# Optimization experiments

Hardware: AMD Instinct MI355X
Metric: run time of the kernel (lower is better)

The kernel has to match this reference:

```python
import jax, jax.numpy as jnp
import numpy as np

N, E, G = 100000, 3200000, 128
F, H = 9, 64


def _lin(key, fan_in, fan_out):
    s = 1.0 / np.sqrt(fan_in)
    k1, k2 = jax.random.split(key)
    W = jax.random.uniform(k1, (fan_in, fan_out), minval=-s, maxval=s, dtype=jnp.float32)
    b = jax.random.uniform(k2, (fan_out,), minval=-s, maxval=s, dtype=jnp.float32)
    return W, b


def setup_inputs() -> dict:
    key = jax.random.key(0)
    ks = jax.random.split(key, 16)
    x = jax.random.normal(ks[0], (N, F), dtype=jnp.float32)
    edge_index = jax.random.randint(ks[1], (2, E), 0, N, dtype=jnp.int64)
    edge_attr = jax.random.normal(ks[2], (E, 1), dtype=jnp.float32)
    batch = jnp.sort(jax.random.randint(ks[3], (N,), 0, G, dtype=jnp.int64))
    B_total = jax.random.uniform(ks[4], (G,), dtype=jnp.float32)
    terminal_mask = jax.random.randint(ks[5], (N,), 0, 2, dtype=jnp.int32)
    c_cost = jax.random.uniform(ks[6], (N,), dtype=jnp.float32)
    We1, be1 = _lin(ks[7], 1, F)   # GINEConv edge projection edge_dim->in_channels
    W1a, b1a = _lin(ks[8], F, H)
    W1b, b1b = _lin(ks[9], H, H)
    We2, be2 = _lin(ks[10], 1, H)
    W2a, b2a = _lin(ks[11], H, H)
    W2b, b2b = _lin(ks[12], H, H)
    Wr1, br1 = _lin(ks[13], H, H // 2)
    Wr2, br2 = _lin(ks[14], H // 2, 1)
    return dict(x=x, edge_index=edge_index, edge_attr=edge_attr, batch=batch,
                B_total=B_total, terminal_mask=terminal_mask, c_cost=c_cost,
                We1=We1, be1=be1, W1a=W1a, b1a=b1a, W1b=W1b, b1b=b1b,
                We2=We2, be2=be2, W2a=W2a, b2a=b2a, W2b=W2b, b2b=b2b,
                Wr1=Wr1, br1=br1, Wr2=Wr2, br2=br2)


def _gine_conv(h, src, dst, edge_attr, We, be, Wa, ba, Wb, bb):
    # GINEConv (eps=0): nn((1+eps)*x_i + sum_j ReLU(x_j + Lin(edge_attr)))
    ea = edge_attr @ We + be                      # [E, dim]
    msg = jax.nn.relu(h[src] + ea)                # gather + edge fuse + relu
    agg = jax.ops.segment_sum(msg, dst, num_segments=N)  # scatter-add
    z = h + agg
    z = jax.nn.relu(z @ Wa + ba)
    return jax.nn.relu(z @ Wb + bb)


def reference(x, edge_index, edge_attr, batch, B_total, terminal_mask, c_cost,
              We1, be1, W1a, b1a, W1b, b1b, We2, be2, W2a, b2a, W2b, b2b,
              Wr1, br1, Wr2, br2):
    src, dst = edge_index[0], edge_index[1]
    h = _gine_conv(x, src, dst, edge_attr, We1, be1, W1a, b1a, W1b, b1b)
    h = _gine_conv(h, src, dst, edge_attr, We2, be2, W2a, b2a, W2b, b2b)
    pi_raw = jax.nn.sigmoid(jax.nn.relu(h @ Wr1 + br1) @ Wr2 + br2)[:, 0]  # [N]
    pi_raw = pi_raw * (1.0 - terminal_mask.astype(pi_raw.dtype))
    node_expenses = pi_raw * c_cost
    total_expenses = jax.ops.segment_sum(node_expenses, batch, num_segments=B_total.shape[0])
    ratio = jnp.minimum(B_total[batch] / (total_expenses[batch] + 1e-12), 1.0)
    return pi_raw * ratio
```

## Files before the change

kernel.cpp:

```cpp
#include <hip/hip_runtime.h>
#include <hip/hip_fp16.h>
#include <math.h>

#define TPB 256
#define P_BLOCKS 512
#define BSHIFT 8
#define BINS_MAX 512

struct alignas(8)  h2x2 { __half2 a, b; };
struct alignas(16) h2x4 { __half2 a, b, c, d; };

typedef _Float16 f16;
typedef __attribute__((ext_vector_type(8))) _Float16 f16x8;
typedef __attribute__((ext_vector_type(4))) float f32x4;

#define MFMA16(a, b, c) __builtin_amdgcn_mfma_f32_16x16x32_f16(a, b, c, 0, 0, 0)

__global__ void __launch_bounds__(256) k_bhist(const int* __restrict__ dst,
                                               int* __restrict__ counts, int E, int B) {
  __shared__ int h[BINS_MAX];
  int t = threadIdx.x, blk = blockIdx.x;
  for (int i = t; i < B; i += TPB) h[i] = 0;
  __syncthreads();
  int chunk = (E + P_BLOCKS - 1) / P_BLOCKS;
  int s = blk * chunk, e = min(E, s + chunk);
  for (int i = s + t; i < e; i += TPB)
    atomicAdd(&h[__builtin_nontemporal_load(&dst[i]) >> BSHIFT], 1);
  __syncthreads();
  for (int i = t; i < B; i += TPB) counts[i * P_BLOCKS + blk] = h[i];
}

__global__ void k_scan_block(const int* __restrict__ deg, int* __restrict__ offs,
                             int* __restrict__ bsums, int n) {
  __shared__ int lds[256];
  int t = threadIdx.x, b = blockIdx.x;
  int base = b * 1024 + t * 4;
  int v0 = (base + 0 < n) ? deg[base + 0] : 0;
  int v1 = (base + 1 < n) ? deg[base + 1] : 0;
  int v2 = (base + 2 < n) ? deg[base + 2] : 0;
  int v3 = (base + 3 < n) ? deg[base + 3] : 0;
  int s = v0 + v1 + v2 + v3;
  lds[t] = s;
  __syncthreads();
  int acc = s;
  for (int off = 1; off < 256; off <<= 1) {
    int x = (t >= off) ? lds[t - off] : 0;
    __syncthreads();
    acc += x;
    lds[t] = acc;
    __syncthreads();
  }
  int excl = acc - s;
  if (base + 0 < n) offs[base + 0] = excl;
  if (base + 1 < n) offs[base + 1] = excl + v0;
  if (base + 2 < n) offs[base + 2] = excl + v0 + v1;
  if (base + 3 < n) offs[base + 3] = excl + v0 + v1 + v2;
  if (t == 255) bsums[b] = acc;
}

__global__ void k_scan_mid(int* __restrict__ bsums, int nb) {
  __shared__ int lds[256];
  int t = threadIdx.x;
  int v = (t < nb) ? bsums[t] : 0;
  lds[t] = v;
  __syncthreads();
  int acc = v;
  for (int off = 1; off < 256; off <<= 1) {
    int x = (t >= off) ? lds[t - off] : 0;
    __syncthreads();
    acc += x;
    lds[t] = acc;
    __syncthreads();
  }
  if (t < nb) bsums[t] = acc - v;
}

__global__ void k_scan_add(int* __restrict__ offs, const int* __restrict__ bsums,
                           int n, int total) {
  int t = threadIdx.x, b = blockIdx.x;
  int add = bsums[b];
  int base = b * 1024 + t * 4;
#pragma unroll
  for (int j = 0; j < 4; ++j)
    if (base + j < n) offs[base + j] += add;
  if (b == 0 && t == 0) offs[n] = total;
}

__global__ void __launch_bounds__(256) k_bfill(const int* __restrict__ src,
                                               const int* __restrict__ dst,
                                               const float* __restrict__ attr,
                                               const int* __restrict__ offs,
                                               int2* __restrict__ ebuf, int E, int B) {
  __shared__ int cur[BINS_MAX];
  int t = threadIdx.x, blk = blockIdx.x;
  for (int i = t; i < B; i += TPB) cur[i] = offs[i * P_BLOCKS + blk];
  __syncthreads();
  int chunk = (E + P_BLOCKS - 1) / P_BLOCKS;
  int s = blk * chunk, e = min(E, s + chunk);
#pragma unroll 4
  for (int i = s + t; i < e; i += TPB) {
    int d = __builtin_nontemporal_load(&dst[i]);
    int sv = __builtin_nontemporal_load(&src[i]);
    float av = __builtin_nontemporal_load(&attr[i]);
    int bin = d >> BSHIFT;
    int pos = atomicAdd(&cur[bin], 1);
    ebuf[pos] = make_int2((sv << BSHIFT) | (d & ((1 << BSHIFT) - 1)), __float_as_int(av));
  }
}

__global__ void __launch_bounds__(256) k_bsort(const long long* __restrict__ ebuf,
                                               const int* __restrict__ offs,
                                               int2* __restrict__ csr,
                                               int* __restrict__ noffs,
                                               int N, int E) {
  __shared__ int hist[256];
  __shared__ int cursor[256];
  __shared__ int sc[256];
  int t = threadIdx.x, bkt = blockIdx.x;
  hist[t] = 0;
  __syncthreads();
  int s = offs[bkt * P_BLOCKS], e = offs[(bkt + 1) * P_BLOCKS];
#pragma unroll 4
  for (int i = s + t; i < e; i += TPB) {
    long long pv = __builtin_nontemporal_load(&ebuf[i]);
    int key = (int)(unsigned int)(pv & 0xffffffffLL);
    atomicAdd(&hist[key & 255], 1);
  }
  __syncthreads();
  int v = hist[t];
  int acc = v;
  sc[t] = v;
  __syncthreads();
  for (int off = 1; off < 256; off <<= 1) {
    int x = (t >= off) ? sc[t - off] : 0;
    __syncthreads();
    acc += x;
    sc[t] = acc;
    __syncthreads();
  }
  int base = s + acc - v;
  cursor[t] = base;
  int n = (bkt << BSHIFT) + t;
  if (n < N) noffs[n] = base;
  if (bkt == 0 && t == 0) noffs[N] = E;
  __syncthreads();
#pragma unroll 4
  for (int i = s + t; i < e; i += TPB) {
    long long pv = __builtin_nontemporal_load(&ebuf[i]);
    int key = (int)(unsigned int)(pv & 0xffffffffLL);
    int attr = (int)(unsigned int)(((unsigned long long)pv) >> 32);
    int pos = atomicAdd(&cursor[key & 255], 1);
    csr[pos] = make_int2(((unsigned int)key) >> BSHIFT, attr);
  }
}

__global__ void __launch_bounds__(256) k_agg1(
    const float* __restrict__ x, const int2* __restrict__ csr,
    const int* __restrict__ noffs, const float* __restrict__ We1,
    const float* __restrict__ be1, float* __restrict__ u1, int N) {
  int t = blockIdx.x * TPB + threadIdx.x;
  int node = t >> 4, f = t & 15;
  if (node >= N || f >= 9) return;
  int o0 = noffs[node], o1 = noffs[node + 1];
  float we = We1[f], be = be1[f];
  float acc = 0.f;
  int e = o0;
  for (; e + 3 < o1; e += 4) {
    int2 p0 = csr[e], p1 = csr[e + 1], p2 = csr[e + 2], p3 = csr[e + 3];
    float v0 = x[p0.x * 9 + f] + fmaf(__int_as_float(p0.y), we, be);
    float v1 = x[p1.x * 9 + f] + fmaf(__int_as_float(p1.y), we, be);
    float v2 = x[p2.x * 9 + f] + fmaf(__int_as_float(p2.y), we, be);
    float v3 = x[p3.x * 9 + f] + fmaf(__int_as_float(p3.y), we, be);
    acc += fmaxf(v0, 0.f) + fmaxf(v1, 0.f) + fmaxf(v2, 0.f) + fmaxf(v3, 0.f);
  }
  for (; e < o1; ++e) {
    int2 p = csr[e];
    acc += fmaxf(x[p.x * 9 + f] + fmaf(__int_as_float(p.y), we, be), 0.f);
  }
  u1[node * 9 + f] = x[node * 9 + f] + acc;
}

__global__ void __launch_bounds__(256) k_agg2(
    const __half* __restrict__ h1, const long long* __restrict__ csr,
    const int* __restrict__ noffs, const float* __restrict__ We2,
    const float* __restrict__ be2, float* __restrict__ u2, int N) {
  int gt = blockIdx.x * TPB + threadIdx.x;
  int node = gt >> 6;
  if (node >= N) return;
  int lane = gt & 63;
  int q = lane >> 3, c = lane & 7;
  float4 weA = *(const float4*)&We2[c * 8];
  float4 weB = *(const float4*)&We2[c * 8 + 4];
  float4 beA = *(const float4*)&be2[c * 8];
  float4 beB = *(const float4*)&be2[c * 8 + 4];
  int o0 = noffs[node], o1 = noffs[node + 1];
  float a0 = 0.f, a1 = 0.f, a2 = 0.f, a3 = 0.f, a4 = 0.f, a5 = 0.f, a6 = 0.f, a7 = 0.f;

#define AGG2_ACC(pv, v)                                                      \
  {                                                                          \
    float ea = __int_as_float((int)(unsigned int)(((unsigned long long)(pv)) >> 32)); \
    float2 f0 = __half22float2((v).a), f1 = __half22float2((v).b);           \
    float2 f2 = __half22float2((v).c), f3 = __half22float2((v).d);           \
    a0 += fmaxf(f0.x + fmaf(ea, weA.x, beA.x), 0.f);                         \
    a1 += fmaxf(f0.y + fmaf(ea, weA.y, beA.y), 0.f);                         \
    a2 += fmaxf(f1.x + fmaf(ea, weA.z, beA.z), 0.f);                         \
    a3 += fmaxf(f1.y + fmaf(ea, weA.w, beA.w), 0.f);                         \
    a4 += fmaxf(f2.x + fmaf(ea, weB.x, beB.x), 0.f);                         \
    a5 += fmaxf(f2.y + fmaf(ea, weB.y, beB.y), 0.f);                         \
    a6 += fmaxf(f3.x + fmaf(ea, weB.z, beB.z), 0.f);                         \
    a7 += fmaxf(f3.y + fmaf(ea, weB.w, beB.w), 0.f);                         \
  }

#define AGG2_ACCM(pv, v, m)                                                  \
  {                                                                          \
    float ea = __int_as_float((int)(unsigned int)(((unsigned long long)(pv)) >> 32)); \
    float2 f0 = __half22float2((v).a), f1 = __half22float2((v).b);           \
    float2 f2 = __half22float2((v).c), f3 = __half22float2((v).d);           \
    a0 += (m) ? fmaxf(f0.x + fmaf(ea, weA.x, beA.x), 0.f) : 0.f;             \
    a1 += (m) ? fmaxf(f0.y + fmaf(ea, weA.y, beA.y), 0.f) : 0.f;             \
    a2 += (m) ? fmaxf(f1.x + fmaf(ea, weA.z, beA.z), 0.f) : 0.f;             \
    a3 += (m) ? fmaxf(f1.y + fmaf(ea, weA.w, beA.w), 0.f) : 0.f;             \
    a4 += (m) ? fmaxf(f2.x + fmaf(ea, weB.x, beB.x), 0.f) : 0.f;             \
    a5 += (m) ? fmaxf(f2.y + fmaf(ea, weB.y, beB.y), 0.f) : 0.f;             \
    a6 += (m) ? fmaxf(f3.x + fmaf(ea, weB.z, beB.z), 0.f) : 0.f;             \
    a7 += (m) ? fmaxf(f3.y + fmaf(ea, weB.w, beB.w), 0.f) : 0.f;             \
  }

  int e = o0;
  for (; e + 32 <= o1; e += 32) {
    long long pv0 = __builtin_nontemporal_load(&csr[e + q]);
    long long pv1 = __builtin_nontemporal_load(&csr[e + 8 + q]);
    long long pv2 = __builtin_nontemporal_load(&csr[e + 16 + q]);
    long long pv3 = __builtin_nontemporal_load(&csr[e + 24 + q]);
    h2x4 v0 = *(const h2x4*)(h1 + (size_t)(int)(unsigned int)(pv0 & 0xffffffffLL) * 64 + c * 8);
    h2x4 v1 = *(const h2x4*)(h1 + (size_t)(int)(unsigned int)(pv1 & 0xffffffffLL) * 64 + c * 8);
    h2x4 v2 = *(const h2x4*)(h1 + (size_t)(int)(unsigned int)(pv2 & 0xffffffffLL) * 64 + c * 8);
    h2x4 v3 = *(const h2x4*)(h1 + (size_t)(int)(unsigned int)(pv3 & 0xffffffffLL) * 64 + c * 8);
    AGG2_ACC(pv0, v0); AGG2_ACC(pv1, v1); AGG2_ACC(pv2, v2); AGG2_ACC(pv3, v3);
  }
  if (e < o1) {
    int last = o1 - 1;
    int i0 = e + q;      bool m0 = i0 < o1; i0 = m0 ? i0 : last;
    int i1 = e + 8 + q;  bool m1 = i1 < o1; i1 = m1 ? i1 : last;
    int i2 = e + 16 + q; bool m2 = i2 < o1; i2 = m2 ? i2 : last;
    int i3 = e + 24 + q; bool m3 = i3 < o1; i3 = m3 ? i3 : last;
    long long pv0 = __builtin_nontemporal_load(&csr[i0]);
    long long pv1 = __builtin_nontemporal_load(&csr[i1]);
    long long pv2 = __builtin_nontemporal_load(&csr[i2]);
    long long pv3 = __builtin_nontemporal_load(&csr[i3]);
    h2x4 v0 = *(const h2x4*)(h1 + (size_t)(int)(unsigned int)(pv0 & 0xffffffffLL) * 64 + c * 8);
    h2x4 v1 = *(const h2x4*)(h1 + (size_t)(int)(unsigned int)(pv1 & 0xffffffffLL) * 64 + c * 8);
    h2x4 v2 = *(const h2x4*)(h1 + (size_t)(int)(unsigned int)(pv2 & 0xffffffffLL) * 64 + c * 8);
    h2x4 v3 = *(const h2x4*)(h1 + (size_t)(int)(unsigned int)(pv3 & 0xffffffffLL) * 64 + c * 8);
    AGG2_ACCM(pv0, v0, m0); AGG2_ACCM(pv1, v1, m1);
    AGG2_ACCM(pv2, v2, m2); AGG2_ACCM(pv3, v3, m3);
  }
#undef AGG2_ACC
#undef AGG2_ACCM

  a0 += __shfl_xor(a0, 8, 64); a0 += __shfl_xor(a0, 16, 64); a0 += __shfl_xor(a0, 32, 64);
  a1 += __shfl_xor(a1, 8, 64); a1 += __shfl_xor(a1, 16, 64); a1 += __shfl_xor(a1, 32, 64);
  a2 += __shfl_xor(a2, 8, 64); a2 += __shfl_xor(a2, 16, 64); a2 += __shfl_xor(a2, 32, 64);
  a3 += __shfl_xor(a3, 8, 64); a3 += __shfl_xor(a3, 16, 64); a3 += __shfl_xor(a3, 32, 64);
  a4 += __shfl_xor(a4, 8, 64); a4 += __shfl_xor(a4, 16, 64); a4 += __shfl_xor(a4, 32, 64);
  a5 += __shfl_xor(a5, 8, 64); a5 += __shfl_xor(a5, 16, 64); a5 += __shfl_xor(a5, 32, 64);
  a6 += __shfl_xor(a6, 8, 64); a6 += __shfl_xor(a6, 16, 64); a6 += __shfl_xor(a6, 32, 64);
  a7 += __shfl_xor(a7, 8, 64); a7 += __shfl_xor(a7, 16, 64); a7 += __shfl_xor(a7, 32, 64);

  if (q == 0) {
    h2x4 sf = *(const h2x4*)(h1 + (size_t)node * 64 + c * 8);
    float2 s0 = __half22float2(sf.a), s1 = __half22float2(sf.b);
    float2 s2 = __half22float2(sf.c), s3 = __half22float2(sf.d);
    float4 oA, oB;
    oA.x = s0.x + a0; oA.y = s0.y + a1; oA.z = s1.x + a2; oA.w = s1.y + a3;
    oB.x = s2.x + a4; oB.y = s2.y + a5; oB.z = s3.x + a6; oB.w = s3.y + a7;
    *(float4*)&u2[(size_t)node * 64 + c * 8] = oA;
    *(float4*)&u2[(size_t)node * 64 + c * 8 + 4] = oB;
  }
}

__global__ void __launch_bounds__(256) k_mlp9(
    const float* __restrict__ uin, const float* __restrict__ Wa,
    const float* __restrict__ ba, const float* __restrict__ Wb,
    const float* __restrict__ bb, __half* __restrict__ hout, int N) {
  constexpr int KIN = 9;
  __shared__ float ls_in[64 * KIN];
  __shared__ float ls_z[64 * 65];
  __shared__ float ls_w[64 * 64];
  __shared__ float ls_b[128];
  const int t = threadIdx.x;
  const int n0 = blockIdx.x * 64;

  for (int i = t; i < 64 * KIN; i += TPB) {
    int r = i / KIN, c = i % KIN;
    int g = n0 + r;
    ls_in[i] = (g < N) ? uin[g * KIN + c] : 0.f;
  }
  for (int i = t; i < KIN * 64; i += TPB) ls_w[i] = Wa[i];
  if (t < 64) { ls_b[t] = ba[t]; ls_b[64 + t] = bb[t]; }
  __syncthreads();

  const int of = (t & 15) * 4, nb = (t >> 4) * 4;
  float acc[4][4];
#pragma unroll
  for (int i = 0; i < 4; ++i)
#pragma unroll
    for (int j = 0; j < 4; ++j) acc[i][j] = 0.f;

  for (int k = 0; k < KIN; ++k) {
    float4 w = *(const float4*)&ls_w[k * 64 + of];
#pragma unroll
    for (int ni = 0; ni < 4; ++ni) {
      float uv = ls_in[(nb + ni) * KIN + k];
      acc[ni][0] += uv * w.x; acc[ni][1] += uv * w.y;
      acc[ni][2] += uv * w.z; acc[ni][3] += uv * w.w;
    }
  }
#pragma unroll
  for (int ni = 0; ni < 4; ++ni)
#pragma unroll
    for (int oi = 0; oi < 4; ++oi)
      ls_z[(nb + ni) * 65 + of + oi] = fmaxf(acc[ni][oi] + ls_b[of + oi], 0.f);
  __syncthreads();
  for (int i = t; i < 4096; i += TPB) ls_w[i] = Wb[i];
  __syncthreads();

#pragma unroll
  for (int i = 0; i < 4; ++i)
#pragma unroll
    for (int j = 0; j < 4; ++j) acc[i][j] = 0.f;
  for (int k = 0; k < 64; ++k) {
    float4 w = *(const float4*)&ls_w[k * 64 + of];
#pragma unroll
    for (int ni = 0; ni < 4; ++ni) {
      float zv = ls_z[(nb + ni) * 65 + k];
      acc[ni][0] += zv * w.x; acc[ni][1] += zv * w.y;
      acc[ni][2] += zv * w.z; acc[ni][3] += zv * w.w;
    }
  }
#pragma unroll
  for (int ni = 0; ni < 4; ++ni) {
    int n = n0 + nb + ni;
    if (n < N) {
      float ox = fmaxf(acc[ni][0] + ls_b[64 + of + 0], 0.f);
      float oy = fmaxf(acc[ni][1] + ls_b[64 + of + 1], 0.f);
      float oz = fmaxf(acc[ni][2] + ls_b[64 + of + 2], 0.f);
      float ow = fmaxf(acc[ni][3] + ls_b[64 + of + 3], 0.f);
      h2x2 hv;
      hv.a = __float22half2_rn(make_float2(ox, oy));
      hv.b = __float22half2_rn(make_float2(oz, ow));
      *(h2x2*)(hout + (size_t)n * 64 + of) = hv;
    }
  }
}

__device__ __forceinline__ void splitf8(const float* v, f16x8& h, f16x8& l) {
#pragma unroll
  for (int j = 0; j < 8; ++j) {
    float x = v[j];
    f16 hh = (f16)x;
    h[j] = hh;
    l[j] = (f16)(x - (float)hh);
  }
}

__device__ __forceinline__ void pack_w(const float* __restrict__ W, int Ntiles, int nslots,
                                       f16* hi, f16* lo, int t) {
  int lane = t & 63;
  int kg = lane >> 4, m = lane & 15;
  int Nout = Ntiles * 16;
  for (int s = t >> 6; s < nslots; s += 4) {
    int ks = s / Ntiles, nt = s - ks * Ntiles;
    int kbase = ks * 32 + kg * 8;
    int n = nt * 16 + m;
    float v[8];
#pragma unroll
    for (int j = 0; j < 8; ++j) v[j] = W[(kbase + j) * Nout + n];
    f16x8 h, l;
    splitf8(v, h, l);
    *(f16x8*)&hi[(s * 64 + lane) * 8] = h;
    *(f16x8*)&lo[(s * 64 + lane) * 8] = l;
  }
}

__global__ void __launch_bounds__(256) k_mlp_ro(
    const float* __restrict__ uin, const float* __restrict__ Wa,
    const float* __restrict__ ba, const float* __restrict__ Wb,
    const float* __restrict__ bb, const float* __restrict__ Wr1,
    const float* __restrict__ br1, const float* __restrict__ Wr2,
    const float* __restrict__ br2, const int* __restrict__ tmask,
    float* __restrict__ pi, int N) {
  __shared__ __align__(16) f16 wf1h[4096], wf1l[4096];
  __shared__ __align__(16) f16 wf2h[4096], wf2l[4096];
  __shared__ __align__(16) f16 wfrh[2048], wfrl[2048];
  __shared__ float ls_z[64 * 65];
  __shared__ float ls_ba[64], ls_bb[64], ls_br1[32], ls_w2[32];
  const int t = threadIdx.x;
  const int n0 = blockIdx.x * 64;

  pack_w(Wa, 4, 8, wf1h, wf1l, t);
  pack_w(Wb, 4, 8, wf2h, wf2l, t);
  pack_w(Wr1, 2, 4, wfrh, wfrl, t);
  if (t < 64) { ls_ba[t] = ba[t]; ls_bb[t] = bb[t]; }
  else if (t < 96) { ls_br1[t - 64] = br1[t - 64]; ls_w2[t - 64] = Wr2[t - 64]; }
  __syncthreads();

  const int w = t >> 6, lane = t & 63;
  const int m = lane & 15, kg = lane >> 4;

  int row = n0 + w * 16 + m;
  row = min(row, N - 1);
  const float* ar = uin + (size_t)row * 64 + kg * 8;
  float av0[8], av1[8];
  {
    f32x4 p0 = *(const f32x4*)ar;
    f32x4 p1 = *(const f32x4*)(ar + 4);
    f32x4 p2 = *(const f32x4*)(ar + 32);
    f32x4 p3 = *(const f32x4*)(ar + 36);
#pragma unroll
    for (int j = 0; j < 4; ++j) {
      av0[j] = p0[j]; av0[4 + j] = p1[j];
      av1[j] = p2[j]; av1[4 + j] = p3[j];
    }
  }
  f16x8 a0h, a0l, a1h, a1l;
  splitf8(av0, a0h, a0l);
  splitf8(av1, a1h, a1l);

  f32x4 acc[4];
#pragma unroll
  for (int nt = 0; nt < 4; ++nt) { f32x4 z4 = {0.f, 0.f, 0.f, 0.f}; acc[nt] = z4; }
#pragma unroll
  for (int nt = 0; nt < 4; ++nt) {
#pragma unroll
    for (int ks = 0; ks < 2; ++ks) {
      int s = ks * 4 + nt;
      f16x8 bh = *(const f16x8*)&wf1h[(s * 64 + lane) * 8];
      f16x8 bl = *(const f16x8*)&wf1l[(s * 64 + lane) * 8];
      f16x8 ah = ks ? a1h : a0h;
      f16x8 al = ks ? a1l : a0l;
      acc[nt] = MFMA16(ah, bh, acc[nt]);
      acc[nt] = MFMA16(al, bh, acc[nt]);
      acc[nt] = MFMA16(ah, bl, acc[nt]);
    }
  }
#pragma unroll
  for (int nt = 0; nt < 4; ++nt)
#pragma unroll
    for (int r = 0; r < 4; ++r)
      ls_z[(w * 16 + kg * 4 + r) * 65 + nt * 16 + m] = fmaxf(acc[nt][r] + ls_ba[nt * 16 + m], 0.f);
  __syncthreads();

  const float* zr = &ls_z[(size_t)(w * 16 + m) * 65 + kg * 8];
  {
    float zv0[8], zv1[8];
#pragma unroll
    for (int j = 0; j < 8; ++j) { zv0[j] = zr[j]; zv1[j] = zr[32 + j]; }
    splitf8(zv0, a0h, a0l);
    splitf8(zv1, a1h, a1l);
  }
#pragma unroll
  for (int nt = 0; nt < 4; ++nt) { f32x4 z4 = {0.f, 0.f, 0.f, 0.f}; acc[nt] = z4; }
#pragma unroll
  for (int nt = 0; nt < 4; ++nt) {
#pragma unroll
    for (int ks = 0; ks < 2; ++ks) {
      int s = ks * 4 + nt;
      f16x8 bh = *(const f16x8*)&wf2h[(s * 64 + lane) * 8];
      f16x8 bl = *(const f16x8*)&wf2l[(s * 64 + lane) * 8];
      f16x8 ah = ks ? a1h : a0h;
      f16x8 al = ks ? a1l : a0l;
      acc[nt] = MFMA16(ah, bh, acc[nt]);
      acc[nt] = MFMA16(al, bh, acc[nt]);
      acc[nt] = MFMA16(ah, bl, acc[nt]);
    }
  }
  __syncthreads();
#pragma unroll
  for (int nt = 0; nt < 4; ++nt)
#pragma unroll
    for (int r = 0; r < 4; ++r)
      ls_z[(w * 16 + kg * 4 + r) * 65 + nt * 16 + m] = fmaxf(acc[nt][r] + ls_bb[nt * 16 + m], 0.f);
  __syncthreads();

  {
    float zv0[8], zv1[8];
#pragma unroll
    for (int j = 0; j < 8; ++j) { zv0[j] = zr[j]; zv1[j] = zr[32 + j]; }
    splitf8(zv0, a0h, a0l);
    splitf8(zv1, a1h, a1l);
  }
  f32x4 accr[2];
#pragma unroll
  for (int nt = 0; nt < 2; ++nt) { f32x4 z4 = {0.f, 0.f, 0.f, 0.f}; accr[nt] = z4; }
#pragma unroll
  for (int nt = 0; nt < 2; ++nt) {
#pragma unroll
    for (int ks = 0; ks < 2; ++ks) {
      int s = ks * 2 + nt;
      f16x8 bh = *(const f16x8*)&wfrh[(s * 64 + lane) * 8];
      f16x8 bl = *(const f16x8*)&wfrl[(s * 64 + lane) * 8];
      f16x8 ah = ks ? a1h : a0h;
      f16x8 al = ks ? a1l : a0l;
      accr[nt] = MFMA16(ah, bh, accr[nt]);
      accr[nt] = MFMA16(al, bh, accr[nt]);
      accr[nt] = MFMA16(ah, bl, accr[nt]);
    }
  }
  float b2 = br2[0];
#pragma unroll
  for (int r = 0; r < 4; ++r) {
    float v0 = fmaxf(accr[0][r] + ls_br1[m], 0.f) * ls_w2[m];
    float v1 = fmaxf(accr[1][r] + ls_br1[16 + m], 0.f) * ls_w2[16 + m];
    float tr = v0 + v1;
    tr += __shfl_xor(tr, 1, 64);
    tr += __shfl_xor(tr, 2, 64);
    tr += __shfl_xor(tr, 4, 64);
    tr += __shfl_xor(tr, 8, 64);
    if (m == 0) {
      int node = n0 + w * 16 + kg * 4 + r;
      if (node < N) {
        float sg = 1.f / (1.f + expf(-(tr + b2)));
        pi[node] = sg * (1.f - (float)tmask[node]);
      }
    }
  }
}

__global__ void k_grpsum(const float* __restrict__ pi, const float* __restrict__ c_cost,
                         const int* __restrict__ batch, float* __restrict__ exp_tot, int N) {
  __shared__ float lsf[256];
  __shared__ int lsi[256];
  int t = threadIdx.x;
  int i = blockIdx.x * TPB + t;
  bool valid = i < N;
  int g = valid ? batch[i] : 0;
  float v = valid ? pi[i] * c_cost[i] : 0.f;
  lsi[t] = valid ? g : 0x7fffffff;
  __syncthreads();
  for (int s = 128; s > 0; s >>= 1) { if (t < s) lsi[t] = min(lsi[t], lsi[t + s]); __syncthreads(); }
  int gmin = lsi[0];
  __syncthreads();
  lsi[t] = valid ? g : -1;
  __syncthreads();
  for (int s = 128; s > 0; s >>= 1) { if (t < s) lsi[t] = max(lsi[t], lsi[t + s]); __syncthreads(); }
  int gmax = lsi[0];
  __syncthreads();
  for (int gg = gmin; gg <= gmax; ++gg) {
    lsf[t] = (valid && g == gg) ? v : 0.f;
    __syncthreads();
    for (int s = 128; s > 0; s >>= 1) { if (t < s) lsf[t] += lsf[t + s]; __syncthreads(); }
    if (t == 0) atomicAdd(&exp_tot[gg], lsf[0]);
    __syncthreads();
  }
}

__global__ void k_final(const float* __restrict__ pi, const int* __restrict__ batch,
                        const float* __restrict__ B_total, const float* __restrict__ exp_tot,
                        float* __restrict__ out, int N) {
  int i = blockIdx.x * TPB + threadIdx.x;
  if (i < N) {
    int g = batch[i];
    float ratio = fminf(B_total[g] / (exp_tot[g] + 1e-12f), 1.f);
    out[i] = pi[i] * ratio;
  }
}

extern "C" void kernel_launch(void* const* d_in, const int* in_sizes, int n_in,
                              void* d_out, int out_size, void* d_ws, size_t ws_size,
                              hipStream_t stream) {
  const float* x     = (const float*)d_in[0];
  const int*   ei    = (const int*)d_in[1];
  const float* eattr = (const float*)d_in[2];
  const int*   batch = (const int*)d_in[3];
  const float* Btot  = (const float*)d_in[4];
  const int*   tmask = (const int*)d_in[5];
  const float* ccost = (const float*)d_in[6];
  const float* We1 = (const float*)d_in[7],  *be1 = (const float*)d_in[8];
  const float* W1a = (const float*)d_in[9],  *b1a = (const float*)d_in[10];
  const float* W1b = (const float*)d_in[11], *b1b = (const float*)d_in[12];
  const float* We2 = (const float*)d_in[13], *be2 = (const float*)d_in[14];
  const float* W2a = (const float*)d_in[15], *b2a = (const float*)d_in[16];
  const float* W2b = (const float*)d_in[17], *b2b = (const float*)d_in[18];
  const float* Wr1 = (const float*)d_in[19], *br1 = (const float*)d_in[20];
  const float* Wr2 = (const float*)d_in[21], *br2 = (const float*)d_in[22];
  float* out = (float*)d_out;

  const int N = in_sizes[0] / 9;
  const int E = in_sizes[2];
  const int G = in_sizes[4];
  const int* src = ei;
  const int* dst = ei + E;
  const int B = (N + (1 << BSHIFT) - 1) >> BSHIFT;
  const int nscan = B * P_BLOCKS;

  size_t cur = 0;
  auto alloc = [&](size_t elems) { size_t r = cur; cur += elems; cur = (cur + 63) & ~(size_t)63; return r; };
  char* wsb = (char*)d_ws;
  size_t o_exp    = alloc(G);
  size_t o_counts = alloc(nscan);
  size_t o_offs   = alloc(nscan + 1);
  size_t o_bsums  = alloc(256);
  size_t o_noffs  = alloc(N + 1);
  size_t o_csr    = alloc(2 * (size_t)E);
  size_t e_or_h   = (2 * (size_t)E > (size_t)N * 32) ? 2 * (size_t)E : (size_t)N * 32;
  size_t o_ebuf   = alloc(e_or_h);
  size_t o_u1     = alloc((size_t)N * 9);
  size_t o_u2     = alloc((size_t)N * 64);
  size_t o_pi     = alloc(N);
  (void)ws_size;

  float* exp_t  = (float*)wsb + o_exp;
  int*   counts = (int*)wsb + o_counts;
  int*   offs   = (int*)wsb + o_offs;
  int*   bsums  = (int*)wsb + o_bsums;
  int*   noffs  = (int*)wsb + o_noffs;
  int2*  csr    = (int2*)((int*)wsb + o_csr);
  int2*  ebuf   = (int2*)((int*)wsb + o_ebuf);
  __half* h1h   = (__half*)((int*)wsb + o_ebuf);
  float* u1     = (float*)wsb + o_u1;
  float* u2     = (float*)wsb + o_u2;
  float* pi     = (float*)wsb + o_pi;

  (void)hipMemsetAsync(exp_t, 0, (size_t)G * 4, stream);

  const int nb = (nscan + 1023) / 1024;

  k_bhist<<<P_BLOCKS, TPB, 0, stream>>>(dst, counts, E, B);
  k_scan_block<<<nb, TPB, 0, stream>>>(counts, offs, bsums, nscan);
  k_scan_mid<<<1, 256, 0, stream>>>(bsums, nb);
  k_scan_add<<<nb, TPB, 0, stream>>>(offs, bsums, nscan, E);
  k_bfill<<<P_BLOCKS, TPB, 0, stream>>>(src, dst, eattr, offs, ebuf, E, B);
  k_bsort<<<B, TPB, 0, stream>>>((const long long*)ebuf, offs, csr, noffs, N, E);

  k_agg1<<<((size_t)N * 16 + TPB - 1) / TPB, TPB, 0, stream>>>(x, csr, noffs, We1, be1, u1, N);
  k_mlp9<<<(N + 63) / 64, TPB, 0, stream>>>(u1, W1a, b1a, W1b, b1b, h1h, N);

  k_agg2<<<((size_t)N * 64 + TPB - 1) / TPB, TPB, 0, stream>>>(h1h, (const long long*)csr, noffs, We2, be2, u2, N);
  k_mlp_ro<<<(N + 63) / 64, TPB, 0, stream>>>(u2, W2a, b2a, W2b, b2b, Wr1, br1, Wr2, br2, tmask, pi, N);

  k_grpsum<<<(N + TPB - 1) / TPB, TPB, 0, stream>>>(pi, ccost, batch, exp_t, N);
  k_final<<<(N + TPB - 1) / TPB, TPB, 0, stream>>>(pi, batch, Btot, exp_t, out, N);
}
```

Baseline: 425.8 us.

## Port layer-1 MLP to split-fp16 MFMA and pack aggregation math into float2

The first-layer node MLP (9->64->64) is rewritten from a scalar LDS-tiled FP32 GEMM to MFMA 16x16x32 f16 instructions, splitting inputs and weights into hi/lo halves to keep near-fp32 accuracy. Separately, the layer-2 edge aggregation switches to two-wide float vectors so the compiler can emit packed FP32 fma/max/add. The MFMA path cuts scalar FMA work but adds split overhead and per-element half stores, and packed math depends on compiler codegen.

After: 419.2 us. Within noise of the previous version (-1.5%).

```diff
diff --git a/kernel.cpp b/kernel.cpp
--- a/kernel.cpp
+++ b/kernel.cpp
@@ -13,6 +13,7 @@
 typedef _Float16 f16;
 typedef __attribute__((ext_vector_type(8))) _Float16 f16x8;
 typedef __attribute__((ext_vector_type(4))) float f32x4;
+typedef __attribute__((ext_vector_type(2))) float f32x2;
 
 #define MFMA16(a, b, c) __builtin_amdgcn_mfma_f32_16x16x32_f16(a, b, c, 0, 0, 0)
 
@@ -189,41 +190,42 @@
   if (node >= N) return;
   int lane = gt & 63;
   int q = lane >> 3, c = lane & 7;
-  float4 weA = *(const float4*)&We2[c * 8];
-  float4 weB = *(const float4*)&We2[c * 8 + 4];
-  float4 beA = *(const float4*)&be2[c * 8];
-  float4 beB = *(const float4*)&be2[c * 8 + 4];
+  f32x2 weP[4], beP[4];
+#pragma unroll
+  for (int p = 0; p < 4; ++p) {
+    weP[p] = *(const f32x2*)&We2[c * 8 + p * 2];
+    beP[p] = *(const f32x2*)&be2[c * 8 + p * 2];
+  }
   int o0 = noffs[node], o1 = noffs[node + 1];
-  float a0 = 0.f, a1 = 0.f, a2 = 0.f, a3 = 0.f, a4 = 0.f, a5 = 0.f, a6 = 0.f, a7 = 0.f;
+  f32x2 A0 = {0.f, 0.f}, A1 = {0.f, 0.f}, A2 = {0.f, 0.f}, A3 = {0.f, 0.f};
+  const f32x2 z2 = {0.f, 0.f};
 
 #define AGG2_ACC(pv, v)                                                      \
   {                                                                          \
-    float ea = __int_as_float((int)(unsigned int)(((unsigned long long)(pv)) >> 32)); \
-    float2 f0 = __half22float2((v).a), f1 = __half22float2((v).b);           \
-    float2 f2 = __half22float2((v).c), f3 = __half22float2((v).d);           \
-    a0 += fmaxf(f0.x + fmaf(ea, weA.x, beA.x), 0.f);                         \
-    a1 += fmaxf(f0.y + fmaf(ea, weA.y, beA.y), 0.f);                         \
-    a2 += fmaxf(f1.x + fmaf(ea, weA.z, beA.z), 0.f);                         \
-    a3 += fmaxf(f1.y + fmaf(ea, weA.w, beA.w), 0.f);                         \
-    a4 += fmaxf(f2.x + fmaf(ea, weB.x, beB.x), 0.f);                         \
-    a5 += fmaxf(f2.y + fmaf(ea, weB.y, beB.y), 0.f);                         \
-    a6 += fmaxf(f3.x + fmaf(ea, weB.z, beB.z), 0.f);                         \
-    a7 += fmaxf(f3.y + fmaf(ea, weB.w, beB.w), 0.f);                         \
-  }
-
-#define AGG2_ACCM(pv, v, m)                                                  \
+    float eaf = __int_as_float((int)(unsigned int)(((unsigned long long)(pv)) >> 32)); \
+    f32x2 ea2 = {eaf, eaf};                                                  \
+    float2 q0 = __half22float2((v).a), q1 = __half22float2((v).b);           \
+    float2 q2 = __half22float2((v).c), q3 = __half22float2((v).d);           \
+    f32x2 g0 = {q0.x, q0.y}, g1 = {q1.x, q1.y};                              \
+    f32x2 g2 = {q2.x, q2.y}, g3 = {q3.x, q3.y};                              \
+    A0 += __builtin_elementwise_max(g0 + __builtin_elementwise_fma(ea2, weP[0], beP[0]), z2); \
+    A1 += __builtin_elementwise_max(g1 + __builtin_elementwise_fma(ea2, weP[1], beP[1]), z2); \
+    A2 += __builtin_elementwise_max(g2 + __builtin_elementwise_fma(ea2, weP[2], beP[2]), z2); \
+    A3 += __builtin_elementwise_max(g3 + __builtin_elementwise_fma(ea2, weP[3], beP[3]), z2); \
+  }
+
+#define AGG2_ACCM(pv, v, mk)                                                 \
   {                                                                          \
-    float ea = __int_as_float((int)(unsigned int)(((unsigned long long)(pv)) >> 32)); \
-    float2 f0 = __half22float2((v).a), f1 = __half22float2((v).b);           \
-    float2 f2 = __half22float2((v).c), f3 = __half22float2((v).d);           \
-    a0 += (m) ? fmaxf(f0.x + fmaf(ea, weA.x, beA.x), 0.f) : 0.f;             \
-    a1 += (m) ? fmaxf(f0.y + fmaf(ea, weA.y, beA.y), 0.f) : 0.f;             \
-    a2 += (m) ? fmaxf(f1.x + fmaf(ea, weA.z, beA.z), 0.f) : 0.f;             \
-    a3 += (m) ? fmaxf(f1.y + fmaf(ea, weA.w, beA.w), 0.f) : 0.f;             \
-    a4 += (m) ? fmaxf(f2.x + fmaf(ea, weB.x, beB.x), 0.f) : 0.f;             \
-    a5 += (m) ? fmaxf(f2.y + fmaf(ea, weB.y, beB.y), 0.f) : 0.f;             \
-    a6 += (m) ? fmaxf(f3.x + fmaf(ea, weB.z, beB.z), 0.f) : 0.f;             \
-    a7 += (m) ? fmaxf(f3.y + fmaf(ea, weB.w, beB.w), 0.f) : 0.f;             \
+    float eaf = __int_as_float((int)(unsigned int)(((unsigned long long)(pv)) >> 32)); \
+    f32x2 ea2 = {eaf, eaf};                                                  \
+    float2 q0 = __half22float2((v).a), q1 = __half22float2((v).b);           \
+    float2 q2 = __half22float2((v).c), q3 = __half22float2((v).d);           \
+    f32x2 g0 = {q0.x, q0.y}, g1 = {q1.x, q1.y};                              \
+    f32x2 g2 = {q2.x, q2.y}, g3 = {q3.x, q3.y};                              \
+    A0 += (mk) ? __builtin_elementwise_max(g0 + __builtin_elementwise_fma(ea2, weP[0], beP[0]), z2) : z2; \
+    A1 += (mk) ? __builtin_elementwise_max(g1 + __builtin_elementwise_fma(ea2, weP[1], beP[1]), z2) : z2; \
+    A2 += (mk) ? __builtin_elementwise_max(g2 + __builtin_elementwise_fma(ea2, weP[2], beP[2]), z2) : z2; \
+    A3 += (mk) ? __builtin_elementwise_max(g3 + __builtin_elementwise_fma(ea2, weP[3], beP[3]), z2) : z2; \
   }
 
   int e = o0;
@@ -258,6 +260,9 @@
 #undef AGG2_ACC
 #undef AGG2_ACCM
 
+  float a0 = A0.x, a1 = A0.y, a2 = A1.x, a3 = A1.y;
+  float a4 = A2.x, a5 = A2.y, a6 = A3.x, a7 = A3.y;
+
   a0 += __shfl_xor(a0, 8, 64); a0 += __shfl_xor(a0, 16, 64); a0 += __shfl_xor(a0, 32, 64);
   a1 += __shfl_xor(a1, 8, 64); a1 += __shfl_xor(a1, 16, 64); a1 += __shfl_xor(a1, 32, 64);
   a2 += __shfl_xor(a2, 8, 64); a2 += __shfl_xor(a2, 16, 64); a2 += __shfl_xor(a2, 32, 64);
@@ -276,81 +281,6 @@
     oB.x = s2.x + a4; oB.y = s2.y + a5; oB.z = s3.x + a6; oB.w = s3.y + a7;
     *(float4*)&u2[(size_t)node * 64 + c * 8] = oA;
     *(float4*)&u2[(size_t)node * 64 + c * 8 + 4] = oB;
-  }
-}
-
-__global__ void __launch_bounds__(256) k_mlp9(
-    const float* __restrict__ uin, const float* __restrict__ Wa,
-    const float* __restrict__ ba, const float* __restrict__ Wb,
-    const float* __restrict__ bb, __half* __restrict__ hout, int N) {
-  constexpr int KIN = 9;
-  __shared__ float ls_in[64 * KIN];
-  __shared__ float ls_z[64 * 65];
-  __shared__ float ls_w[64 * 64];
-  __shared__ float ls_b[128];
-  const int t = threadIdx.x;
-  const int n0 = blockIdx.x * 64;
-
-  for (int i = t; i < 64 * KIN; i += TPB) {
-    int r = i / KIN, c = i % KIN;
-    int g = n0 + r;
-    ls_in[i] = (g < N) ? uin[g * KIN + c] : 0.f;
-  }
-  for (int i = t; i < KIN * 64; i += TPB) ls_w[i] = Wa[i];
-  if (t < 64) { ls_b[t] = ba[t]; ls_b[64 + t] = bb[t]; }
-  __syncthreads();
-
-  const int of = (t & 15) * 4, nb = (t >> 4) * 4;
-  float acc[4][4];
-#pragma unroll
-  for (int i = 0; i < 4; ++i)
-#pragma unroll
-    for (int j = 0; j < 4; ++j) acc[i][j] = 0.f;
-
-  for (int k = 0; k < KIN; ++k) {
-    float4 w = *(const float4*)&ls_w[k * 64 + of];
-#pragma unroll
-    for (int ni = 0; ni < 4; ++ni) {
-      float uv = ls_in[(nb + ni) * KIN + k];
-      acc[ni][0] += uv * w.x; acc[ni][1] += uv * w.y;
-      acc[ni][2] += uv * w.z; acc[ni][3] += uv * w.w;
-    }
-  }
-#pragma unroll
-  for (int ni = 0; ni < 4; ++ni)
-#pragma unroll
-    for (int oi = 0; oi < 4; ++oi)
-      ls_z[(nb + ni) * 65 + of + oi] = fmaxf(acc[ni][oi] + ls_b[of + oi], 0.f);
-  __syncthreads();
-  for (int i = t; i < 4096; i += TPB) ls_w[i] = Wb[i];
-  __syncthreads();
-
-#pragma unroll
-  for (int i = 0; i < 4; ++i)
-#pragma unroll
-    for (int j = 0; j < 4; ++j) acc[i][j] = 0.f;
-  for (int k = 0; k < 64; ++k) {
-    float4 w = *(const float4*)&ls_w[k * 64 + of];
-#pragma unroll
-    for (int ni = 0; ni < 4; ++ni) {
-      float zv = ls_z[(nb + ni) * 65 + k];
-      acc[ni][0] += zv * w.x; acc[ni][1] += zv * w.y;
-      acc[ni][2] += zv * w.z; acc[ni][3] += zv * w.w;
-    }
-  }
-#pragma unroll
-  for (int ni = 0; ni < 4; ++ni) {
-    int n = n0 + nb + ni;
-    if (n < N) {
-      float ox = fmaxf(acc[ni][0] + ls_b[64 + of + 0], 0.f);
-      float oy = fmaxf(acc[ni][1] + ls_b[64 + of + 1], 0.f);
-      float oz = fmaxf(acc[ni][2] + ls_b[64 + of + 2], 0.f);
-      float ow = fmaxf(acc[ni][3] + ls_b[64 + of + 3], 0.f);
-      h2x2 hv;
-      hv.a = __float22half2_rn(make_float2(ox, oy));
-      hv.b = __float22half2_rn(make_float2(oz, ow));
-      *(h2x2*)(hout + (size_t)n * 64 + of) = hv;
-    }
   }
 }
 
@@ -381,6 +311,100 @@
     *(f16x8*)&hi[(s * 64 + lane) * 8] = h;
     *(f16x8*)&lo[(s * 64 + lane) * 8] = l;
   }
+}
+
+__global__ void __launch_bounds__(256) k_mlp9(
+    const float* __restrict__ uin, const float* __restrict__ Wa,
+    const float* __restrict__ ba, const float* __restrict__ Wb,
+    const float* __restrict__ bb, __half* __restrict__ hout, int N) {
+  __shared__ __align__(16) f16 wf1h[2048], wf1l[2048];
+  __shared__ __align__(16) f16 wf2h[4096], wf2l[4096];
+  __shared__ float ls_z[64 * 65];
+  __shared__ float ls_ba[64], ls_bb[64];
+  const int t = threadIdx.x;
+  const int n0 = blockIdx.x * 64;
+  const int w = t >> 6, lane = t & 63;
+  const int m = lane & 15, kg = lane >> 4;
+
+  {
+    int s = w;
+    int n = s * 16 + m;
+    float v[8];
+#pragma unroll
+    for (int j = 0; j < 8; ++j) {
+      int k = kg * 8 + j;
+      v[j] = (k < 9) ? Wa[k * 64 + n] : 0.f;
+    }
+    f16x8 h, l;
+    splitf8(v, h, l);
+    *(f16x8*)&wf1h[(s * 64 + lane) * 8] = h;
+    *(f16x8*)&wf1l[(s * 64 + lane) * 8] = l;
+  }
+  pack_w(Wb, 4, 8, wf2h, wf2l, t);
+  if (t < 64) { ls_ba[t] = ba[t]; ls_bb[t] = bb[t]; }
+  __syncthreads();
+
+  int row = min(n0 + w * 16 + m, N - 1);
+  float av[8];
+#pragma unroll
+  for (int j = 0; j < 8; ++j) {
+    int k = kg * 8 + j;
+    av[j] = (k < 9) ? uin[(size_t)row * 9 + k] : 0.f;
+  }
+  f16x8 a0h, a0l, a1h, a1l;
+  splitf8(av, a0h, a0l);
+
+  f32x4 acc[4];
+#pragma unroll
+  for (int nt = 0; nt < 4; ++nt) { f32x4 z4 = {0.f, 0.f, 0.f, 0.f}; acc[nt] = z4; }
+#pragma unroll
+  for (int nt = 0; nt < 4; ++nt) {
+    f16x8 bh = *(const f16x8*)&wf1h[(nt * 64 + lane) * 8];
+    f16x8 bl = *(const f16x8*)&wf1l[(nt * 64 + lane) * 8];
+    acc[nt] = MFMA16(a0h, bh, acc[nt]);
+    acc[nt] = MFMA16(a0l, bh, acc[nt]);
+    acc[nt] = MFMA16(a0h, bl, acc[nt]);
+  }
+#pragma unroll
+  for (int nt = 0; nt < 4; ++nt)
+#pragma unroll
+    for (int r = 0; r < 4; ++r)
+      ls_z[(w * 16 + kg * 4 + r) * 65 + nt * 16 + m] = fmaxf(acc[nt][r] + ls_ba[nt * 16 + m], 0.f);
+  __syncthreads();
+
+  const float* zr = &ls_z[(size_t)(w * 16 + m) * 65 + kg * 8];
+  {
+    float zv0[8], zv1[8];
+#pragma unroll
+    for (int j = 0; j < 8; ++j) { zv0[j] = zr[j]; zv1[j] = zr[32 + j]; }
+    splitf8(zv0, a0h, a0l);
+    splitf8(zv1, a1h, a1l);
+  }
+#pragma unroll
+  for (int nt = 0; nt < 4; ++nt) { f32x4 z4 = {0.f, 0.f, 0.f, 0.f}; acc[nt] = z4; }
+#pragma unroll
+  for (int nt = 0; nt < 4; ++nt) {
+#pragma unroll
+    for (int ks = 0; ks < 2; ++ks) {
+      int s = ks * 4 + nt;
+      f16x8 bh = *(const f16x8*)&wf2h[(s * 64 + lane) * 8];
+      f16x8 bl = *(const f16x8*)&wf2l[(s * 64 + lane) * 8];
+      f16x8 ah = ks ? a1h : a0h;
+      f16x8 al = ks ? a1l : a0l;
+      acc[nt] = MFMA16(ah, bh, acc[nt]);
+      acc[nt] = MFMA16(al, bh, acc[nt]);
+      acc[nt] = MFMA16(ah, bl, acc[nt]);
+    }
+  }
+#pragma unroll
+  for (int nt = 0; nt < 4; ++nt)
+#pragma unroll
+    for (int r = 0; r < 4; ++r) {
+      int node = n0 + w * 16 + kg * 4 + r;
+      if (node < N)
+        hout[(size_t)node * 64 + nt * 16 + m] =
+            __float2half(fmaxf(acc[nt][r] + ls_bb[nt * 16 + m], 0.f));
+    }
 }
 
 __global__ void __launch_bounds__(256) k_mlp_ro(
```
